# Kernel optimization log

Hardware: AMD Instinct MI355X
Metric: run time of the kernel (lower is better)

## Reference

```python
import jax, jax.numpy as jnp
import numpy as np
from jax import lax

B, C, T, V = 16, 3, 256, 25
MID = 48
DILS = (1, 2, 3, 4)
NB = len(DILS)
OUT = MID * NB
FH = [10, 100, 10, 1]
CH = [100]
EPS = 1e-5


def setup_inputs() -> dict:
    key = jax.random.key(0)
    ks = iter(jax.random.split(key, 64))
    nrm = lambda shape, s=0.05: jax.random.normal(next(ks), shape, jnp.float32) * s
    inp = {}
    inp['x'] = jax.random.normal(next(ks), (B, C, T, V), jnp.float32)
    # stacked per-timestep branch conv weights: (branch, v, mid, in=V, k=3)
    inp['Wb'] = nrm((NB, V, MID, V, 3))
    inp['bb'] = nrm((NB, V, MID))
    dims = [C] + FH
    for i in range(4):
        inp[f'fw{i}'] = nrm((dims[i + 1], dims[i]))
        inp[f'fb{i}'] = nrm((dims[i + 1],))
        inp[f'fg{i}'] = jnp.ones((dims[i + 1],), jnp.float32)
        inp[f'fbe{i}'] = jnp.zeros((dims[i + 1],), jnp.float32)
    cdims = [V] + CH + [OUT]
    for i in range(2):
        inp[f'cw{i}'] = nrm((cdims[i + 1], cdims[i]))
        inp[f'cb{i}'] = nrm((cdims[i + 1],))
        inp[f'cg{i}'] = jnp.ones((cdims[i + 1],), jnp.float32)
        inp[f'cbe{i}'] = jnp.zeros((cdims[i + 1],), jnp.float32)
    inp['Ww'] = nrm((V, OUT))  # branches_follow 1x1 conv weights (per v)
    inp['bw'] = nrm((V,))
    return inp


def _bn2d(y, g, b):
    m = y.mean((0, 2, 3), keepdims=True)
    v = ((y - m) ** 2).mean((0, 2, 3), keepdims=True)
    return g[None, :, None, None] * (y - m) / jnp.sqrt(v + EPS) + b[None, :, None, None]


def _bn1d(y, g, b):
    m = y.mean((0, 2), keepdims=True)
    v = ((y - m) ** 2).mean((0, 2), keepdims=True)
    return g[None, :, None] * (y - m) / jnp.sqrt(v + EPS) + b[None, :, None]


def reference(x, Wb, bb, fw0, fb0, fg0, fbe0, fw1, fb1, fg1, fbe1,
              fw2, fb2, fg2, fbe2, fw3, fb3, fg3, fbe3,
              cw0, cb0, cg0, cbe0, cw1, cb1, cg1, cbe1, Ww, bw):
    N = B * C
    x_temp = x.reshape(N, T, V).transpose(0, 2, 1)  # (N, V, T)
    # --- branches: 25 convs per branch fused as one big conv (out = V*MID) ---
    outs = []
    for i, d in enumerate(DILS):
        pad = 2 * d  # k + (k-1)(d-1) - 1 with k=3
        kern = Wb[i].reshape(V * MID, V, 3)
        y = lax.conv_general_dilated(x_temp, kern, window_strides=(1,),
                                     padding=[(pad, 0)], rhs_dilation=(d,),
                                     dimension_numbers=('NCH', 'OIH', 'NCH'))
        y = y + bb[i].reshape(V * MID)[None, :, None]  # (N, V*MID, T)
        # torch.cat over the 25 convs along time -> (N, MID, V*T)
        y = y.reshape(N, V, MID, T).transpose(0, 2, 1, 3).reshape(N, MID, V * T)
        outs.append(y)
    predic = jnp.stack(outs)  # (NB, N, MID, V*T)
    predic = predic.transpose(1, 0, 2, 3).reshape(N, NB * MID, V * T)
    predic = predic.reshape(N, -1, T, V).reshape(B, C, OUT, T, V)
    # --- feature branches (1x1 Conv2d + BN + ReLU chain) ---
    h = x
    for w, bi, g, be in ((fw0, fb0, fg0, fbe0), (fw1, fb1, fg1, fbe1),
                         (fw2, fb2, fg2, fbe2), (fw3, fb3, fg3, fbe3)):
        h = jnp.einsum('bctv,oc->botv', h, w) + bi[None, :, None, None]
        h = jax.nn.relu(_bn2d(h, g, be))
    h = h.reshape(-1, T, V).transpose(0, 2, 1).mean(-1, keepdims=True)  # (B, V, 1)
    # --- causal branches (1x1 Conv1d + BN + ReLU) ---
    for w, bi, g, be in ((cw0, cb0, cg0, cbe0), (cw1, cb1, cg1, cbe1)):
        h = jnp.einsum('bcl,oc->bol', h, w) + bi[None, :, None]
        h = jax.nn.relu(_bn1d(h, g, be))
    xg = h[:, :, :, None]  # (B, OUT, 1, 1)
    # --- gate, relu, per-timestep follow convs ---
    predic = predic * xg[:, None]  # (B, C, OUT, T, V)
    predic = jax.nn.relu(predic.reshape(N, OUT, T, V))
    predic_final = jnp.einsum('notv,vo->nvt', predic, Ww) + bw[None, :, None]  # (N, V, T)
    predic_loss = (predic_final[:, :, :-1] - x_temp[:, :, 1:]) ** 2  # MSE, no reduction
    # --- GC pool + regularization ---
    gc_pool = Wb.transpose(0, 2, 1, 3, 4).reshape(OUT, V, V, 3)
    gcw = gc_pool[None] * xg[:, :, :, :, None]  # (B, OUT, V, V, 3)
    lam = jnp.float32(0.01)
    reg = lam * (jnp.sum(jnp.sqrt(jnp.sum(gcw ** 2, axis=(1, 4)))) +
                 jnp.sum(jnp.sqrt(jnp.sum(gcw ** 2, axis=1))))
    gc = gcw.max(axis=1).max(axis=-1)  # (B, V, V)
    return (predic_loss, gc, reg)
```

## Files before the change

### kernel.cpp

```cpp
#include <hip/hip_runtime.h>

#define EPSV 1e-5f

constexpr int kB = 16, kC = 3, kT = 256, kV = 25;
constexpr int kMID = 48, kNB = 4, kOUT = 192, kN = 48;
constexpr int kS  = kB * kT * kV;
constexpr int kTV = kT * kV;

typedef __attribute__((ext_vector_type(8))) short bf16x8;
typedef __attribute__((ext_vector_type(4))) float f32x4;

__device__ __forceinline__ short f2bf(float f) {
  unsigned u = __float_as_uint(f);
  u += 0x7fffu + ((u >> 16) & 1u);
  return (short)(u >> 16);
}
__device__ __forceinline__ float bf2f(short s) {
  return __uint_as_float(((unsigned)(unsigned short)s) << 16);
}
__device__ __forceinline__ float wred(float v) {
  #pragma unroll
  for (int d = 32; d > 0; d >>= 1) v += __shfl_xor(v, d);
  return v;
}


__device__ __forceinline__ void st0_from_xmom(int o, const float* fw0, const float* fb0,
                                              const float* fg0, const float* fbe0,
                                              const float* xmom, float* sc0, float* sh0)
{
  float w0 = fw0[o * 3], w1 = fw0[o * 3 + 1], w2 = fw0[o * 3 + 2], b = fb0[o];
  float Sw = w0 * xmom[0] + w1 * xmom[1] + w2 * xmom[2];
  float Q  = w0*w0*xmom[3] + w1*w1*xmom[6] + w2*w2*xmom[8]
           + 2.f*(w0*w1*xmom[4] + w0*w2*xmom[5] + w1*w2*xmom[7]);
  float mean = (Sw + (float)kS * b) * (1.f / kS);
  float e2   = (Q + 2.f * b * Sw) * (1.f / kS) + b * b;
  float var  = e2 - mean * mean;
  float sc   = fg0[o] * rsqrtf(var + EPSV);
  sc0[o] = sc; sh0[o] = fbe0[o] - mean * sc;
}

__device__ __forceinline__ void st1_analytic(int o, const float* w1p, const float* fg1,
                                             const float* fbe1, const float* H0MOM,
                                             float* sc1, float* sh1)
{
  float wr[10]; float S = 0.f, Q = 0.f;
  #pragma unroll
  for (int c = 0; c < 10; c++) { wr[c] = w1p[o*12+c]; S = fmaf(wr[c], H0MOM[c], S); }
  int idx = 10;
  #pragma unroll
  for (int c = 0; c < 10; c++) {
    Q = fmaf(wr[c]*wr[c], H0MOM[idx], Q); idx++;
    #pragma unroll
    for (int cp = c + 1; cp < 10; cp++) { Q = fmaf(2.f*wr[c]*wr[cp], H0MOM[idx], Q); idx++; }
  }
  float b = w1p[o*12+10];
  float mean = (S + (float)kS * b) * (1.f / kS);
  float e2   = (Q + 2.f * b * S) * (1.f / kS) + b * b;
  float var  = e2 - mean * mean;
  float sc   = fg1[o] * rsqrtf(var + EPSV);
  sc1[o] = sc; sh1[o] = fbe1[o] - mean * sc;
}

__global__ __launch_bounds__(128) void prep_xmom(
    const float* __restrict__ x, const float* __restrict__ Wb,
    short* __restrict__ XSG, short* __restrict__ WBBF, float* __restrict__ xmom)
{
  __shared__ float red[9];
  const int tid = threadIdx.x;
  const int gtid = blockIdx.x * 128 + tid;

  for (int j = gtid; j < 48 * 10560; j += 102400) {
    int n = j / 10560, rem = j - n * 10560;
    int row = rem / 40, ci = rem - row * 40;
    short val = 0;
    if (row >= 8 && ci < 25) val = f2bf(x[n * 6400 + (row - 8) * 25 + ci]);
    XSG[j] = val;
  }
  for (int j = gtid; j < 499200; j += 102400) {
    int g = j / 4992, rem = j - g * 4992;
    int m = rem / 104, kk = rem - m * 104;
    int k = kk >> 5, ci = kk & 31;
    short val = 0;
    if (ci < 25 && kk < 96) val = f2bf(Wb[g * 3600 + m * 75 + ci * 3 + k]);
    WBBF[j] = val;
  }

  if (tid < 9) red[tid] = 0.f;
  __syncthreads();
  const int s = gtid;
  const int b = s / kTV, r = s - b * kTV;
  const float x0 = x[(b * 3 + 0) * kTV + r];
  const float x1 = x[(b * 3 + 1) * kTV + r];
  const float x2 = x[(b * 3 + 2) * kTV + r];
  const float pm[9] = {x0, x1, x2, x0*x0, x0*x1, x0*x2, x1*x1, x1*x2, x2*x2};
  #pragma unroll
  for (int k = 0; k < 9; k++) {
    float t = wred(pm[k]);
    if ((tid & 63) == 0) atomicAdd(&red[k], t);
  }
  __syncthreads();
  if (tid < 9) atomicAdd(&xmom[tid], red[tid]);
}

__global__ __launch_bounds__(128) void h0mom_kernel(
    const float* __restrict__ x,
    const float* __restrict__ fw0, const float* __restrict__ fb0,
    const float* __restrict__ fg0, const float* __restrict__ fbe0,
    const float* __restrict__ xmom, float* __restrict__ h0mom)
{
  __shared__ __align__(16) float w0p[40];
  __shared__ float sc0[10], sh0[10];
  __shared__ float red[65];
  const int tid = threadIdx.x;
  for (int j = tid; j < 40; j += 128) {
    int o = j >> 2, c = j & 3;
    w0p[j] = (c < 3) ? fw0[o * 3 + c] : fb0[o];
  }
  if (tid < 10) st0_from_xmom(tid, fw0, fb0, fg0, fbe0, xmom, sc0, sh0);
  if (tid < 65) red[tid] = 0.f;
  __syncthreads();
  const int s = blockIdx.x * 128 + tid;
  const int b = s / kTV, r = s - b * kTV;
  const float x0 = x[(b * 3 + 0) * kTV + r];
  const float x1 = x[(b * 3 + 1) * kTV + r];
  const float x2 = x[(b * 3 + 2) * kTV + r];
  float h0[10];
  #pragma unroll
  for (int o = 0; o < 10; o++) {
    const float4 w = *(const float4*)&w0p[o * 4];
    float y = fmaf(x0, w.x, fmaf(x1, w.y, fmaf(x2, w.z, w.w)));
    h0[o] = fmaxf(fmaf(y, sc0[o], sh0[o]), 0.f);
  }
  int idx = 0;
  #pragma unroll
  for (int c = 0; c < 10; c++) {
    float t = wred(h0[c]);
    if ((tid & 63) == 0) atomicAdd(&red[idx], t);
    idx++;
  }
  #pragma unroll
  for (int c = 0; c < 10; c++)
    #pragma unroll
    for (int cp = c; cp < 10; cp++) {
      float t = wred(h0[c] * h0[cp]);
      if ((tid & 63) == 0) atomicAdd(&red[idx], t);
      idx++;
    }
  __syncthreads();
  if (tid < 65) atomicAdd(&h0mom[tid], red[tid]);
}

__global__ __launch_bounds__(128) void st2acc(
    const float* __restrict__ x,
    const float* __restrict__ fw0, const float* __restrict__ fb0,
    const float* __restrict__ fg0, const float* __restrict__ fbe0,
    const float* __restrict__ fw1, const float* __restrict__ fb1,
    const float* __restrict__ fg1, const float* __restrict__ fbe1,
    const float* __restrict__ fw2, const float* __restrict__ fb2,
    const float* __restrict__ xmom, const float* __restrict__ h0mom,
    short* __restrict__ accout, float* __restrict__ st2out)
{
  __shared__ __align__(16) float w0p[40];
  __shared__ __align__(16) float w1p[1200];
  __shared__ __align__(16) float w2t[1200];
  __shared__ float b2s[10];
  __shared__ float sc0[10], sh0[10], sc1[100], sh1[100];
  __shared__ float red[20];
  const int tid = threadIdx.x;

  for (int j = tid; j < 40; j += 128) {
    int o = j >> 2, c = j & 3;
    w0p[j] = (c < 3) ? fw0[o * 3 + c] : fb0[o];
  }
  for (int j = tid; j < 1200; j += 128) {
    int o = j / 12, c = j - o * 12;
    w1p[j] = (c < 10) ? fw1[o * 10 + c] : (c == 10 ? fb1[o] : 0.f);
  }
  for (int j = tid; j < 1000; j += 128) {
    int jj = j / 100, c = j - jj * 100;
    w2t[c * 12 + jj] = fw2[j];
  }
  for (int c = tid; c < 100; c += 128) { w2t[c * 12 + 10] = 0.f; w2t[c * 12 + 11] = 0.f; }
  if (tid < 10) {
    b2s[tid] = fb2[tid];
    st0_from_xmom(tid, fw0, fb0, fg0, fbe0, xmom, sc0, sh0);
  }
  if (tid < 20) red[tid] = 0.f;
  __syncthreads();
  if (tid < 100) st1_analytic(tid, w1p, fg1, fbe1, h0mom, sc1, sh1);
  __syncthreads();

  const int s = blockIdx.x * 128 + tid;
  const int b = s / kTV, r = s - b * kTV;
  const float x0 = x[(b * 3 + 0) * kTV + r];
  const float x1 = x[(b * 3 + 1) * kTV + r];
  const float x2 = x[(b * 3 + 2) * kTV + r];
  float h0[10];
  #pragma unroll
  for (int o = 0; o < 10; o++) {
    const float4 w = *(const float4*)&w0p[o * 4];
    float y = fmaf(x0, w.x, fmaf(x1, w.y, fmaf(x2, w.z, w.w)));
    h0[o] = fmaxf(fmaf(y, sc0[o], sh0[o]), 0.f);
  }
  float acc[10];
  #pragma unroll
  for (int o = 0; o < 10; o++) acc[o] = b2s[o];
  #pragma unroll 4
  for (int o = 0; o < 100; o++) {
    const float4 wa = *(const float4*)&w1p[o * 12];
    const float4 wb = *(const float4*)&w1p[o * 12 + 4];
    const float4 wc = *(const float4*)&w1p[o * 12 + 8];
    float a = wc.z;
    a = fmaf(h0[0], wa.x, a); a = fmaf(h0[1], wa.y, a);
    a = fmaf(h0[2], wa.z, a); a = fmaf(h0[3], wa.w, a);
    a = fmaf(h0[4], wb.x, a); a = fmaf(h0[5], wb.y, a);
    a = fmaf(h0[6], wb.z, a); a = fmaf(h0[7], wb.w, a);
    a = fmaf(h0[8], wc.x, a); a = fmaf(h0[9], wc.y, a);
    const float h1 = fmaxf(fmaf(a, sc1[o], sh1[o]), 0.f);
    const float4 va = *(const float4*)&w2t[o * 12];
    const float4 vb = *(const float4*)&w2t[o * 12 + 4];
    const float4 vc = *(const float4*)&w2t[o * 12 + 8];
    acc[0] = fmaf(h1, va.x, acc[0]); acc[1] = fmaf(h1, va.y, acc[1]);
    acc[2] = fmaf(h1, va.z, acc[2]); acc[3] = fmaf(h1, va.w, acc[3]);
    acc[4] = fmaf(h1, vb.x, acc[4]); acc[5] = fmaf(h1, vb.y, acc[5]);
    acc[6] = fmaf(h1, vb.z, acc[6]); acc[7] = fmaf(h1, vb.w, acc[7]);
    acc[8] = fmaf(h1, vc.x, acc[8]); acc[9] = fmaf(h1, vc.y, acc[9]);
  }
  #pragma unroll
  for (int o = 0; o < 10; o++) accout[o * kS + s] = f2bf(acc[o]);
  #pragma unroll
  for (int o = 0; o < 10; o++) {
    float s1 = wred(acc[o]), s2 = wred(acc[o] * acc[o]);
    if ((tid & 63) == 0) { atomicAdd(&red[2 * o], s1); atomicAdd(&red[2 * o + 1], s2); }
  }
  __syncthreads();
  if (tid < 20) atomicAdd(&st2out[tid], red[tid]);
}

__global__ __launch_bounds__(128) void h2y3(
    const short* __restrict__ ACC,
    const float* __restrict__ fg2, const float* __restrict__ fbe2,
    const float* __restrict__ fw3, const float* __restrict__ fb3,
    const float* __restrict__ st2,
    short* __restrict__ y3out, float* __restrict__ st3out)
{
  __shared__ float sc2[10], sh2[10], w3s[12];
  __shared__ float red[2];
  const int tid = threadIdx.x;
  if (tid < 10) {
    float m  = st2[2 * tid] * (1.f / kS);
    float vr = st2[2 * tid + 1] * (1.f / kS) - m * m;
    float sc = fg2[tid] * rsqrtf(vr + EPSV);
    sc2[tid] = sc; sh2[tid] = fbe2[tid] - m * sc;
  }
  if (tid < 12) w3s[tid] = (tid < 10) ? fw3[tid] : (tid == 10 ? fb3[0] : 0.f);
  if (tid < 2) red[tid] = 0.f;
  __syncthreads();
  const int s = blockIdx.x * 128 + tid;
  float y3 = w3s[10];
  #pragma unroll
  for (int o = 0; o < 10; o++) {
    float h2 = fmaxf(fmaf(bf2f(ACC[o * kS + s]), sc2[o], sh2[o]), 0.f);
    y3 = fmaf(h2, w3s[o], y3);
  }
  y3out[s] = f2bf(y3);
  float s1 = wred(y3), s2 = wred(y3 * y3);
  if ((tid & 63) == 0) { atomicAdd(&red[0], s1); atomicAdd(&red[1], s2); }
  __syncthreads();
  if (tid < 2) atomicAdd(&st3out[tid], red[tid]);
}

__global__ __launch_bounds__(128) void poolpass(
    const short* __restrict__ y3,
    const float* __restrict__ fg3, const float* __restrict__ fbe3,
    const float* __restrict__ st3, float* __restrict__ hp)
{
  __shared__ float scsh[2];
  __shared__ float poolp[25];
  const int tid = threadIdx.x;
  if (tid == 0) {
    float m  = st3[0] * (1.f / kS);
    float vr = st3[1] * (1.f / kS) - m * m;
    float sc = fg3[0] * rsqrtf(vr + EPSV);
    scsh[0] = sc; scsh[1] = fbe3[0] - m * sc;
  }
  if (tid < 25) poolp[tid] = 0.f;
  __syncthreads();
  const int s = blockIdx.x * 128 + tid;
  const int b = s / kTV, r = s - b * kTV;
  float h3 = fmaxf(fmaf(bf2f(y3[s]), scsh[0], scsh[1]), 0.f);
  atomicAdd(&poolp[r % 25], h3);
  __syncthreads();
  if (tid < 25) atomicAdd(&hp[b * 25 + tid], poolp[tid]);
}

__global__ __launch_bounds__(256) void head_kernel(
    const float* __restrict__ hp,
    const float* __restrict__ cw0, const float* __restrict__ cb0,
    const float* __restrict__ cg0, const float* __restrict__ cbe0,
    const float* __restrict__ cw1, const float* __restrict__ cb1,
    const float* __restrict__ cg1, const float* __restrict__ cbe1,
    float* __restrict__ xg, float* __restrict__ xgT)
{
  __shared__ float hpl[400];
  __shared__ float y1[100 * 16];
  __shared__ float y2l[192 * 16];
  const int tid = threadIdx.x;
  for (int j = tid; j < 400; j += 256) hpl[j] = hp[j] * (1.f / kT);
  __syncthreads();
  for (int j = tid; j < 1600; j += 256) {
    int o = j >> 4, b = j & 15;
    float acc = cb0[o];
    for (int v = 0; v < 25; v++) acc = fmaf(hpl[b * 25 + v], cw0[o * 25 + v], acc);
    y1[o * 16 + b] = acc;
  }
  __syncthreads();
  if (tid < 100) {
    float s1 = 0.f, s2 = 0.f;
    for (int b = 0; b < 16; b++) { float val = y1[tid * 16 + b]; s1 += val; s2 += val * val; }
    float m = s1 * (1.f / 16), vr = s2 * (1.f / 16) - m * m;
    float scale = cg0[tid] * rsqrtf(vr + EPSV);
    float shift = cbe0[tid] - m * scale;
    for (int b = 0; b < 16; b++)
      y1[tid * 16 + b] = fmaxf(fmaf(y1[tid * 16 + b], scale, shift), 0.f);
  }
  __syncthreads();
  for (int j = tid; j < 3072; j += 256) {
    int o = j >> 4, b = j & 15;
    float acc = cb1[o];
    for (int c = 0; c < 100; c++) acc = fmaf(y1[c * 16 + b], cw1[o * 100 + c], acc);
    y2l[o * 16 + b] = acc;
  }
  __syncthreads();
  if (tid < 192) {
    float s1 = 0.f, s2 = 0.f;
    for (int b = 0; b < 16; b++) { float val = y2l[tid * 16 + b]; s1 += val; s2 += val * val; }
    float m = s1 * (1.f / 16), vr = s2 * (1.f / 16) - m * m;
    float scale = cg1[tid] * rsqrtf(vr + EPSV);
    float shift = cbe1[tid] - m * scale;
    for (int b = 0; b < 16; b++) {
      float r = fmaxf(fmaf(y2l[tid * 16 + b], scale, shift), 0.f);
      xg[b * 192 + tid]  = r;
      xgT[tid * 16 + b]  = r;
    }
  }
}

__global__ __launch_bounds__(64) void gw_gcreg(
    const float* __restrict__ Wb, const float* __restrict__ Ww,
    const float* __restrict__ XG, const float* __restrict__ XGT,
    float* __restrict__ GW, float* __restrict__ gc_out, float* __restrict__ reg_out)
{
  const int tid = threadIdx.x;
  const int bid = blockIdx.x;
  if (bid < 80) {
    for (int j = bid * 64 + tid; j < 76800; j += 5120) {
      int bidx = j / 4800, rem = j - bidx * 4800;
      int vp = rem / 192, o = rem - vp * 192;
      GW[bidx * 5100 + vp * 204 + o] = XG[bidx * 192 + o] * Ww[vp * 192 + o];
    }
    return;
  }
  __shared__ float sW[576];
  __shared__ float sG[192 * 17];
  const int u = bid - 80;
  const int v1 = u / 25, v2 = u - v1 * 25;
  for (int j = tid; j < 3072; j += 64) {
    int o = j >> 4, bq = j & 15;
    sG[o * 17 + bq] = XGT[j];
  }
  for (int p = tid; p < 192; p += 64) {
    int i = p / 48, m = p - i * 48;
    const float* src = Wb + ((i * 25 + v1) * 48 + m) * 75 + v2 * 3;
    sW[p * 3 + 0] = src[0]; sW[p * 3 + 1] = src[1]; sW[p * 3 + 2] = src[2];
  }
  __syncthreads();
  const int b = tid & 15, c = tid >> 4;
  float s0 = 0.f, s1 = 0.f, s2 = 0.f, mx = -3.0e38f;
  #pragma unroll 4
  for (int o = c * 48; o < c * 48 + 48; o++) {
    float g = sG[o * 17 + b];
    float a0 = sW[o * 3] * g, a1 = sW[o * 3 + 1] * g, a2 = sW[o * 3 + 2] * g;
    s0 = fmaf(a0, a0, s0);
    s1 = fmaf(a1, a1, s1);
    s2 = fmaf(a2, a2, s2);
    mx = fmaxf(mx, fmaxf(fmaxf(a0, a1), a2));
  }
  s0 += __shfl_xor(s0, 16); s0 += __shfl_xor(s0, 32);
  s1 += __shfl_xor(s1, 16); s1 += __shfl_xor(s1, 32);
  s2 += __shfl_xor(s2, 16); s2 += __shfl_xor(s2, 32);
  mx = fmaxf(mx, __shfl_xor(mx, 16)); mx = fmaxf(mx, __shfl_xor(mx, 32));
  float contrib = 0.f;
  if (c == 0) {
    gc_out[(b * 25 + v1) * 25 + v2] = mx;
    contrib = sqrtf(s0 + s1 + s2) + sqrtf(s0) + sqrtf(s1) + sqrtf(s2);
  }
  #pragma unroll
  for (int d = 1; d < 16; d <<= 1) contrib += __shfl_xor(contrib, d);
  if (tid == 0) atomicAdd(reg_out, 0.01f * contrib);
}

__global__ __launch_bounds__(256) void conv_fuse_mfma(
    const short* __restrict__ XSG, const short* __restrict__ WBBF,
    const float* __restrict__ GW, const float* __restrict__ x,
    const float* __restrict__ bb, const float* __restrict__ bw,
    float* __restrict__ out_loss)
{
  __shared__ __align__(16) short xs[264 * 40];
  __shared__ __align__(16) short As[48 * 104];
  __shared__ __align__(16) float gw[25 * 204];
  __shared__ float bbl[192], bwl[32];

  const int tid = threadIdx.x;
  const int v = blockIdx.x % 25, n = blockIdx.x / 25;
  const int bidx = n / 3;

  {
    const uint4* src = (const uint4*)(XSG + n * 10560);
    uint4* dst = (uint4*)xs;
    for (int j = tid; j < 1320; j += 256) dst[j] = src[j];
  }
  {
    const float4* src = (const float4*)(GW + bidx * 5100);
    float4* dst = (float4*)gw;
    for (int j = tid; j < 1275; j += 256) dst[j] = src[j];
  }
  for (int j = tid; j < 192; j += 256) {
    int i = j / 48, m = j - i * 48;
    bbl[j] = bb[(i * 25 + v) * 48 + m];
  }
  if (tid < 25) bwl[tid] = bw[tid];

  const int lane = tid & 63, w = tid >> 6;
  const int c = lane & 15, q = lane >> 4;

  float accout[4] = {0.f, 0.f, 0.f, 0.f};
  int tarr[4], vparr[4];
  #pragma unroll
  for (int z = 0; z < 4; z++) {
    int t = (w * 4 + z) * 16 + c;
    tarr[z] = t;
    vparr[z] = (v * 256 + t) % 25;
  }

  for (int i = 0; i < 4; i++) {
    __syncthreads();
    {
      const uint4* src = (const uint4*)(WBBF + (i * 25 + v) * 4992);
      uint4* dst = (uint4*)As;
      for (int j = tid; j < 624; j += 256) dst[j] = src[j];
    }
    __syncthreads();

    const int d = i + 1;
    bf16x8 af[3][3];
    #pragma unroll
    for (int mt = 0; mt < 3; mt++)
      #pragma unroll
      for (int s = 0; s < 3; s++)
        af[mt][s] = *(const bf16x8*)&As[(mt * 16 + c) * 104 + s * 32 + q * 8];

    #pragma unroll
    for (int z = 0; z < 4; z++) {
      const int t = tarr[z];
      bf16x8 bfv[3];
      #pragma unroll
      for (int s = 0; s < 3; s++) {
        int row = 8 + t + (s - 2) * d;
        bfv[s] = *(const bf16x8*)&xs[row * 40 + q * 8];
      }
      f32x4 acc[3] = {{0.f,0.f,0.f,0.f},{0.f,0.f,0.f,0.f},{0.f,0.f,0.f,0.f}};
      #pragma unroll
      for (int s = 0; s < 3; s++)
        #pragma unroll
        for (int mt = 0; mt < 3; mt++)
          acc[mt] = __builtin_amdgcn_mfma_f32_16x16x32_bf16(af[mt][s], bfv[s], acc[mt], 0, 0, 0);
      const int vp = vparr[z];
      float aout = 0.f;
      #pragma unroll
      for (int mt = 0; mt < 3; mt++) {
        const int ob = i * 48 + mt * 16 + q * 4;
        const float4 g4 = *(const float4*)&gw[vp * 204 + ob];
        float v0 = fmaxf(acc[mt][0] + bbl[ob + 0], 0.f);
        float v1 = fmaxf(acc[mt][1] + bbl[ob + 1], 0.f);
        float v2 = fmaxf(acc[mt][2] + bbl[ob + 2], 0.f);
        float v3 = fmaxf(acc[mt][3] + bbl[ob + 3], 0.f);
        aout = fmaf(v0, g4.x, aout);
        aout = fmaf(v1, g4.y, aout);
        aout = fmaf(v2, g4.z, aout);
        aout = fmaf(v3, g4.w, aout);
      }
      accout[z] += aout;
    }
  }

  #pragma unroll
  for (int z = 0; z < 4; z++) {
    float a = accout[z];
    a += __shfl_xor(a, 16);
    a += __shfl_xor(a, 32);
    if (q == 0) {
      int flat = v * 256 + tarr[z];
      int tp = flat / 25, vp = flat - tp * 25;
      if (tp < 255) {
        float pf = a + bwl[vp];
        float xn = x[n * 6400 + (tp + 1) * 25 + vp];
        float dd = pf - xn;
        out_loss[(n * 25 + vp) * 255 + tp] = dd * dd;
      }
    }
  }
}

extern "C" void kernel_launch(void* const* d_in, const int* in_sizes, int n_in,
                              void* d_out, int out_size, void* d_ws, size_t ws_size,
                              hipStream_t stream)
{
  const float* x    = (const float*)d_in[0];
  const float* Wb   = (const float*)d_in[1];
  const float* bb   = (const float*)d_in[2];
  const float* fw0  = (const float*)d_in[3];
  const float* fb0  = (const float*)d_in[4];
  const float* fg0  = (const float*)d_in[5];
  const float* fbe0 = (const float*)d_in[6];
  const float* fw1  = (const float*)d_in[7];
  const float* fb1  = (const float*)d_in[8];
  const float* fg1  = (const float*)d_in[9];
  const float* fbe1 = (const float*)d_in[10];
  const float* fw2  = (const float*)d_in[11];
  const float* fb2  = (const float*)d_in[12];
  const float* fg2  = (const float*)d_in[13];
  const float* fbe2 = (const float*)d_in[14];
  const float* fw3  = (const float*)d_in[15];
  const float* fb3  = (const float*)d_in[16];
  const float* fg3  = (const float*)d_in[17];
  const float* fbe3 = (const float*)d_in[18];
  const float* cw0  = (const float*)d_in[19];
  const float* cb0  = (const float*)d_in[20];
  const float* cg0  = (const float*)d_in[21];
  const float* cbe0 = (const float*)d_in[22];
  const float* cw1  = (const float*)d_in[23];
  const float* cb1  = (const float*)d_in[24];
  const float* cg1  = (const float*)d_in[25];
  const float* cbe1 = (const float*)d_in[26];
  const float* Ww   = (const float*)d_in[27];
  const float* bw   = (const float*)d_in[28];

  float* ws  = (float*)d_ws;
  float* out = (float*)d_out;

  float* XMOM  = ws;
  float* H0MOM = ws + 16;
  float* ST2   = ws + 96;
  float* ST3   = ws + 128;
  float* HP    = ws + 208;
  float* XG    = ws + 608;
  float* XGT   = ws + 3680;
  short* ACC   = (short*)(ws + 8192);
  float* GW    = ws + 8192;
  short* Y3    = (short*)(ws + 520192);
  short* WBBF  = (short*)(ws + 571392);
  short* XSG   = (short*)(ws + 820992);

  hipMemsetAsync(ws, 0, 608 * sizeof(float), stream);
  hipMemsetAsync(out + 316000, 0, sizeof(float), stream);

  prep_xmom<<<800, 128, 0, stream>>>(x, Wb, XSG, WBBF, XMOM);
  h0mom_kernel<<<800, 128, 0, stream>>>(x, fw0, fb0, fg0, fbe0, XMOM, H0MOM);
  st2acc<<<800, 128, 0, stream>>>(x, fw0, fb0, fg0, fbe0, fw1, fb1, fg1, fbe1,
      fw2, fb2, XMOM, H0MOM, ACC, ST2);
  h2y3<<<800, 128, 0, stream>>>(ACC, fg2, fbe2, fw3, fb3, ST2, Y3, ST3);
  poolpass<<<800, 128, 0, stream>>>(Y3, fg3, fbe3, ST3, HP);
  head_kernel<<<1, 256, 0, stream>>>(HP, cw0, cb0, cg0, cbe0, cw1, cb1, cg1, cbe1, XG, XGT);
  gw_gcreg<<<705, 64, 0, stream>>>(Wb, Ww, XG, XGT, GW, out + 306000, out + 316000);
  conv_fuse_mfma<<<1200, 256, 0, stream>>>(XSG, WBBF, GW, x, bb, bw, out);
}
```

Before: 177.5 us.

## Fuse pooling into head kernel and compute gated follow weights inside conv

Merges the pooling pass into the single-block head kernel, which now reads the whole y3 buffer with vector loads and accumulates per-(batch,v) sums with shared-memory atomics. The gated follow-conv weight product is computed directly in each conv block instead of by a separate pass writing a global buffer, and the reg zeroing moves into the head kernel. This removes launches and a global round trip, but serializes a large reduction onto one block and adds redundant multiplies per conv block.

```diff
diff --git a/kernel.cpp b/kernel.cpp
--- a/kernel.cpp
+++ b/kernel.cpp
@@ -271,43 +271,45 @@
   if (tid < 2) atomicAdd(&st3out[tid], red[tid]);
 }
 
-__global__ __launch_bounds__(128) void poolpass(
-    const short* __restrict__ y3,
+__global__ __launch_bounds__(256) void head2_kernel(
+    const short* __restrict__ y3, const float* __restrict__ st3,
     const float* __restrict__ fg3, const float* __restrict__ fbe3,
-    const float* __restrict__ st3, float* __restrict__ hp)
+    const float* __restrict__ cw0, const float* __restrict__ cb0,
+    const float* __restrict__ cg0, const float* __restrict__ cbe0,
+    const float* __restrict__ cw1, const float* __restrict__ cb1,
+    const float* __restrict__ cg1, const float* __restrict__ cbe1,
+    float* __restrict__ xg, float* __restrict__ xgT, float* __restrict__ reg_out)
 {
   __shared__ float scsh[2];
-  __shared__ float poolp[25];
+  __shared__ float hpl[400];
+  __shared__ float y1[100 * 16];
+  __shared__ float y2l[192 * 16];
   const int tid = threadIdx.x;
   if (tid == 0) {
+    reg_out[0] = 0.f;
     float m  = st3[0] * (1.f / kS);
     float vr = st3[1] * (1.f / kS) - m * m;
     float sc = fg3[0] * rsqrtf(vr + EPSV);
     scsh[0] = sc; scsh[1] = fbe3[0] - m * sc;
   }
-  if (tid < 25) poolp[tid] = 0.f;
-  __syncthreads();
-  const int s = blockIdx.x * 128 + tid;
-  const int b = s / kTV, r = s - b * kTV;
-  float h3 = fmaxf(fmaf(bf2f(y3[s]), scsh[0], scsh[1]), 0.f);
-  atomicAdd(&poolp[r % 25], h3);
-  __syncthreads();
-  if (tid < 25) atomicAdd(&hp[b * 25 + tid], poolp[tid]);
-}
-
-__global__ __launch_bounds__(256) void head_kernel(
-    const float* __restrict__ hp,
-    const float* __restrict__ cw0, const float* __restrict__ cb0,
-    const float* __restrict__ cg0, const float* __restrict__ cbe0,
-    const float* __restrict__ cw1, const float* __restrict__ cb1,
-    const float* __restrict__ cg1, const float* __restrict__ cbe1,
-    float* __restrict__ xg, float* __restrict__ xgT)
-{
-  __shared__ float hpl[400];
-  __shared__ float y1[100 * 16];
-  __shared__ float y2l[192 * 16];
-  const int tid = threadIdx.x;
-  for (int j = tid; j < 400; j += 256) hpl[j] = hp[j] * (1.f / kT);
+  for (int j = tid; j < 400; j += 256) hpl[j] = 0.f;
+  __syncthreads();
+  {
+    const float sc = scsh[0], sh = scsh[1];
+    for (int it = 0; it < 50; it++) {
+      const int base = (tid * 50 + it) * 8;
+      const bf16x8 v8 = *(const bf16x8*)&y3[base];
+      #pragma unroll
+      for (int e = 0; e < 8; e++) {
+        const int s = base + e;
+        const int b = s / kTV, vv = s % 25;
+        float h3 = fmaxf(fmaf(bf2f(v8[e]), sc, sh), 0.f);
+        atomicAdd(&hpl[b * 25 + vv], h3);
+      }
+    }
+  }
+  __syncthreads();
+  for (int j = tid; j < 400; j += 256) hpl[j] *= (1.f / kT);
   __syncthreads();
   for (int j = tid; j < 1600; j += 256) {
     int o = j >> 4, b = j & 15;
@@ -347,25 +349,14 @@
   }
 }
 
-__global__ __launch_bounds__(64) void gw_gcreg(
-    const float* __restrict__ Wb, const float* __restrict__ Ww,
-    const float* __restrict__ XG, const float* __restrict__ XGT,
-    float* __restrict__ GW, float* __restrict__ gc_out, float* __restrict__ reg_out)
-{
-  const int tid = threadIdx.x;
-  const int bid = blockIdx.x;
-  if (bid < 80) {
-    for (int j = bid * 64 + tid; j < 76800; j += 5120) {
-      int bidx = j / 4800, rem = j - bidx * 4800;
-      int vp = rem / 192, o = rem - vp * 192;
-      GW[bidx * 5100 + vp * 204 + o] = XG[bidx * 192 + o] * Ww[vp * 192 + o];
-    }
-    return;
-  }
+__global__ __launch_bounds__(64) void gcreg_kernel(
+    const float* __restrict__ Wb, const float* __restrict__ XGT,
+    float* __restrict__ gc_out, float* __restrict__ reg_out)
+{
   __shared__ float sW[576];
   __shared__ float sG[192 * 17];
-  const int u = bid - 80;
-  const int v1 = u / 25, v2 = u - v1 * 25;
+  const int tid = threadIdx.x;
+  const int v1 = blockIdx.x / 25, v2 = blockIdx.x % 25;
   for (int j = tid; j < 3072; j += 64) {
     int o = j >> 4, bq = j & 15;
     sG[o * 17 + bq] = XGT[j];
@@ -403,9 +394,9 @@
 
 __global__ __launch_bounds__(256) void conv_fuse_mfma(
     const short* __restrict__ XSG, const short* __restrict__ WBBF,
-    const float* __restrict__ GW, const float* __restrict__ x,
-    const float* __restrict__ bb, const float* __restrict__ bw,
-    float* __restrict__ out_loss)
+    const float* __restrict__ XG, const float* __restrict__ Ww,
+    const float* __restrict__ x, const float* __restrict__ bb,
+    const float* __restrict__ bw, float* __restrict__ out_loss)
 {
   __shared__ __align__(16) short xs[264 * 40];
   __shared__ __align__(16) short As[48 * 104];
@@ -421,10 +412,9 @@
     uint4* dst = (uint4*)xs;
     for (int j = tid; j < 1320; j += 256) dst[j] = src[j];
   }
-  {
-    const float4* src = (const float4*)(GW + bidx * 5100);
-    float4* dst = (float4*)gw;
-    for (int j = tid; j < 1275; j += 256) dst[j] = src[j];
+  for (int j = tid; j < 4800; j += 256) {
+    int vv = j / 192, o = j - vv * 192;
+    gw[vv * 204 + o] = XG[bidx * 192 + o] * Ww[j];
   }
   for (int j = tid; j < 192; j += 256) {
     int i = j / 48, m = j - i * 48;
@@ -554,25 +544,22 @@
   float* H0MOM = ws + 16;
   float* ST2   = ws + 96;
   float* ST3   = ws + 128;
-  float* HP    = ws + 208;
   float* XG    = ws + 608;
   float* XGT   = ws + 3680;
   short* ACC   = (short*)(ws + 8192);
-  float* GW    = ws + 8192;
   short* Y3    = (short*)(ws + 520192);
   short* WBBF  = (short*)(ws + 571392);
   short* XSG   = (short*)(ws + 820992);
 
   hipMemsetAsync(ws, 0, 608 * sizeof(float), stream);
-  hipMemsetAsync(out + 316000, 0, sizeof(float), stream);
 
   prep_xmom<<<800, 128, 0, stream>>>(x, Wb, XSG, WBBF, XMOM);
   h0mom_kernel<<<800, 128, 0, stream>>>(x, fw0, fb0, fg0, fbe0, XMOM, H0MOM);
   st2acc<<<800, 128, 0, stream>>>(x, fw0, fb0, fg0, fbe0, fw1, fb1, fg1, fbe1,
       fw2, fb2, XMOM, H0MOM, ACC, ST2);
   h2y3<<<800, 128, 0, stream>>>(ACC, fg2, fbe2, fw3, fb3, ST2, Y3, ST3);
-  poolpass<<<800, 128, 0, stream>>>(Y3, fg3, fbe3, ST3, HP);
-  head_kernel<<<1, 256, 0, stream>>>(HP, cw0, cb0, cg0, cbe0, cw1, cb1, cg1, cbe1, XG, XGT);
-  gw_gcreg<<<705, 64, 0, stream>>>(Wb, Ww, XG, XGT, GW, out + 306000, out + 316000);
-  conv_fuse_mfma<<<1200, 256, 0, stream>>>(XSG, WBBF, GW, x, bb, bw, out);
-}
+  head2_kernel<<<1, 256, 0, stream>>>(Y3, ST3, fg3, fbe3,
+      cw0, cb0, cg0, cbe0, cw1, cb1, cg1, cbe1, XG, XGT, out + 316000);
+  gcreg_kernel<<<625, 64, 0, stream>>>(Wb, XGT, out + 306000, out + 316000);
+  conv_fuse_mfma<<<1200, 256, 0, stream>>>(XSG, WBBF, XG, Ww, x, bb, bw, out);
+}
```

After: 336.2 us. 1.89x slower.
